# Kernel tuning notes

Hardware: AMD Instinct MI355X
Metric: run time of the kernel (lower is better)

Reference implementation:

```python
import jax, jax.numpy as jnp
import numpy as np

B, E, C = 1024, 512, 16384
MRG, ALPHA, V, K, LAM, TAU = 0.1, 32.0, 100.0, 1.0, 0.1, 1.5


def _l2norm(x):
    # matches torch l2_norm: divide by sqrt(sum(x^2) + 1e-12) row-wise
    n = jnp.sqrt(jnp.sum(x * x, axis=1) + 1e-12)
    return x / n[:, None]


def setup_inputs() -> dict:
    key = jax.random.key(0)
    k1, k2, k3, k4, k5 = jax.random.split(key, 5)
    inputsBatch = _l2norm(jax.random.normal(k1, (B, E), dtype=jnp.float32))
    targetsBatch = jax.random.randint(k2, (B,), 0, C, dtype=jnp.int32)
    # kaiming_normal fan_out on (C, E): std = sqrt(2 / E)
    proxies = jax.random.normal(k3, (C, E), dtype=jnp.float32) * np.sqrt(2.0 / E).astype(np.float32)
    effectiveNum = jax.random.uniform(k4, (C,), dtype=jnp.float32) * 100.0
    learnedSim = jax.random.uniform(k5, (C,), dtype=jnp.float32)
    return {"inputsBatch": inputsBatch, "targetsBatch": targetsBatch,
            "proxies": proxies, "effectiveNum": effectiveNum, "learnedSim": learnedSim}


def reference(inputsBatch, targetsBatch, proxies, effectiveNum, learnedSim):
    nb_classes = proxies.shape[0]
    P = jax.nn.one_hot(targetsBatch, nb_classes, dtype=inputsBatch.dtype)  # [B, C]
    N = 1.0 - P
    proxy_l2 = _l2norm(proxies)
    cos = inputsBatch @ proxy_l2.T  # [B, C]

    classCnt = P.sum(axis=0)                      # [C]
    present = (classCnt > 0).astype(cos.dtype)

    w_base = 1.0 / (1.0 + jnp.log1p(effectiveNum))
    eta = (1.0 + K * (1.0 - learnedSim)) * w_base + LAM
    outlierSim = learnedSim - eta                 # [C]

    # enableFilter=False: mask at positive positions stays 1, so each present
    # class contributes mean(ones)=1 to pos_weight_sum
    pos_weight_sum = jnp.sum(present)

    # negative-position adaptive reweighting (vectorized over the class loop)
    neg_vals = jnp.where(cos < outlierSim[None, :],
                         (1.0 / jnp.maximum(1.0, effectiveNum))[None, :],
                         1.0)                      # [B, C]
    Ncnt = N.sum(axis=0)
    neg_mean = jnp.sum(N * neg_vals, axis=0) / jnp.maximum(Ncnt, 1.0)
    neg_weight_sum = jnp.sum(jnp.where(Ncnt > 0, neg_mean, 0.0))

    mask = jnp.where(N > 0, neg_vals, 1.0)        # 1 at positive entries

    pos_term = jnp.sum(jnp.log1p(jnp.sum(P * jnp.exp(ALPHA * (MRG - cos) * mask), axis=0)))
    neg_term = jnp.sum(jnp.log1p(jnp.sum(N * jnp.exp(ALPHA * (cos + MRG) * mask), axis=0)))

    return pos_term / pos_weight_sum + neg_term / neg_weight_sum
```

## Files before the change

### kernel.cpp

```cpp
#include <hip/hip_runtime.h>
#include <math.h>

#define B_SZ 1024
#define E_SZ 512
#define C_SZ 16384
#define MRG 0.1f
#define ALPHA 32.0f
#define K_HY 1.0f
#define LAM 0.1f

typedef __bf16 bf16;
typedef bf16 bf16x8 __attribute__((ext_vector_type(8)));
typedef float f32x4 __attribute__((ext_vector_type(4)));

__device__ __forceinline__ void async16(const void* g, void* l) {
    __builtin_amdgcn_global_load_lds(
        (const __attribute__((address_space(1))) void*)g,
        (__attribute__((address_space(3))) void*)l,
        16, 0, 0);
}

__global__ void class_scalars(const float* __restrict__ effNum,
                              const float* __restrict__ lSim,
                              float* __restrict__ oSim,
                              float* __restrict__ iEff) {
    int c = blockIdx.x * 256 + threadIdx.x;
    if (c < C_SZ) {
        float en = effNum[c], ls = lSim[c];
        float wb = 1.0f / (1.0f + log1pf(en));
        float eta = (1.0f + K_HY * (1.0f - ls)) * wb + LAM;
        oSim[c] = ls - eta;
        iEff[c] = 1.0f / fmaxf(1.0f, en);
    }
}

__global__ void proxy_norm(const float* __restrict__ proxies, bf16* __restrict__ Pbf) {
    int row = (blockIdx.x * 256 + threadIdx.x) >> 6;
    int lane = threadIdx.x & 63;
    const float* pr = proxies + (size_t)row * E_SZ + lane * 8;
    float4 v0 = *(const float4*)pr;
    float4 v1 = *(const float4*)(pr + 4);
    float ss = v0.x * v0.x + v0.y * v0.y + v0.z * v0.z + v0.w * v0.w +
               v1.x * v1.x + v1.y * v1.y + v1.z * v1.z + v1.w * v1.w;
#pragma unroll
    for (int m = 1; m < 64; m <<= 1) ss += __shfl_xor(ss, m);
    float inv = 1.0f / sqrtf(ss + 1e-12f);
    bf16x8 o;
    o[0] = (bf16)(v0.x * inv); o[1] = (bf16)(v0.y * inv);
    o[2] = (bf16)(v0.z * inv); o[3] = (bf16)(v0.w * inv);
    o[4] = (bf16)(v1.x * inv); o[5] = (bf16)(v1.y * inv);
    o[6] = (bf16)(v1.z * inv); o[7] = (bf16)(v1.w * inv);
    *(bf16x8*)(Pbf + (size_t)row * E_SZ + lane * 8) = o;
}

__global__ void convert_inputs(const float* __restrict__ x, bf16* __restrict__ y) {
    int i = (blockIdx.x * 256 + threadIdx.x) * 8;
    float4 v0 = *(const float4*)(x + i);
    float4 v1 = *(const float4*)(x + i + 4);
    bf16x8 o;
    o[0] = (bf16)v0.x; o[1] = (bf16)v0.y; o[2] = (bf16)v0.z; o[3] = (bf16)v0.w;
    o[4] = (bf16)v1.x; o[5] = (bf16)v1.y; o[6] = (bf16)v1.z; o[7] = (bf16)v1.w;
    *(bf16x8*)(y + i) = o;
}

__global__ void count_targets(const int* __restrict__ tg, int* __restrict__ cnt) {
    int i = blockIdx.x * 256 + threadIdx.x;
    if (i < B_SZ) atomicAdd(&cnt[tg[i]], 1);
}

__global__ __launch_bounds__(256) void gemm_epilogue(
    const bf16* __restrict__ Abf,
    const bf16* __restrict__ Pbf,
    const int* __restrict__ targets,
    const float* __restrict__ oSimA,
    const float* __restrict__ iEffA,
    float* __restrict__ posExp,
    float* __restrict__ negExp,
    float* __restrict__ negVals) {
    __shared__ __align__(16) bf16 Alds[128 * 32];
    __shared__ __align__(16) bf16 Blds[128 * 32];
    __shared__ int tgtLds[128];

    const int tid = threadIdx.x;
    const int wave = tid >> 6, lane = tid & 63;
    const int quad = lane >> 4, l16 = lane & 15;
    const int wRow = (wave >> 1) * 64, wCol = (wave & 1) * 64;
    const int bn0 = blockIdx.x * 128, bm0 = blockIdx.y * 128;

    if (tid < 128) tgtLds[tid] = targets[bm0 + tid];

    f32x4 zero = {0.f, 0.f, 0.f, 0.f};
    f32x4 acc[4][4];
#pragma unroll
    for (int i = 0; i < 4; ++i)
#pragma unroll
        for (int j = 0; j < 4; ++j) acc[i][j] = zero;

    const int ldRow = lane >> 2;
    const int ldK = (lane & 3) * 8;

    const bf16* gA = Abf + (size_t)(bm0 + wave * 32 + ldRow) * E_SZ + ldK;
    const bf16* gB = Pbf + (size_t)(bn0 + wave * 32 + ldRow) * E_SZ + ldK;

    for (int k0 = 0; k0 < E_SZ; k0 += 32) {
        __syncthreads();
#pragma unroll
        for (int j = 0; j < 2; ++j) {
            int chunk = wave * 2 + j;
            async16(gA + (size_t)j * 16 * E_SZ + k0, &Alds[chunk * 512]);
            async16(gB + (size_t)j * 16 * E_SZ + k0, &Blds[chunk * 512]);
        }
        __syncthreads();
        bf16x8 af[4], bff[4];
#pragma unroll
        for (int mi = 0; mi < 4; ++mi)
            af[mi] = *(const bf16x8*)&Alds[(wRow + mi * 16 + l16) * 32 + quad * 8];
#pragma unroll
        for (int ni = 0; ni < 4; ++ni)
            bff[ni] = *(const bf16x8*)&Blds[(wCol + ni * 16 + l16) * 32 + quad * 8];
#pragma unroll
        for (int mi = 0; mi < 4; ++mi)
#pragma unroll
            for (int ni = 0; ni < 4; ++ni)
                acc[mi][ni] = __builtin_amdgcn_mfma_f32_16x16x32_bf16(
                    af[mi], bff[ni], acc[mi][ni], 0, 0, 0);
    }

    int colG[4];
    float oS[4], iE[4];
#pragma unroll
    for (int ni = 0; ni < 4; ++ni) {
        colG[ni] = bn0 + wCol + ni * 16 + l16;
        oS[ni] = oSimA[colG[ni]];
        iE[ni] = iEffA[colG[ni]];
    }
    float negE[4] = {0.f, 0.f, 0.f, 0.f};
    float negV[4] = {0.f, 0.f, 0.f, 0.f};
#pragma unroll
    for (int mi = 0; mi < 4; ++mi) {
#pragma unroll
        for (int r = 0; r < 4; ++r) {
            int rowL = wRow + mi * 16 + quad * 4 + r;
            int tgt = tgtLds[rowL];
#pragma unroll
            for (int ni = 0; ni < 4; ++ni) {
                float cosv = acc[mi][ni][r];
                if (tgt == colG[ni]) {
                    atomicAdd(&posExp[colG[ni]], expf(ALPHA * (MRG - cosv)));
                } else {
                    float nv = (cosv < oS[ni]) ? iE[ni] : 1.0f;
                    negE[ni] += expf(ALPHA * (cosv + MRG) * nv);
                    negV[ni] += nv;
                }
            }
        }
    }
#pragma unroll
    for (int ni = 0; ni < 4; ++ni) {
        float e = negE[ni], v = negV[ni];
        e += __shfl_xor(e, 16); e += __shfl_xor(e, 32);
        v += __shfl_xor(v, 16); v += __shfl_xor(v, 32);
        if (quad == 0) {
            atomicAdd(&negExp[colG[ni]], e);
            atomicAdd(&negVals[colG[ni]], v);
        }
    }
}

__global__ __launch_bounds__(256) void finalize_partial(
    const float* __restrict__ posExp, const float* __restrict__ negExp,
    const float* __restrict__ negVals, const int* __restrict__ cCnt,
    float* __restrict__ acc4) {
    int c = blockIdx.x * 256 + threadIdx.x;
    float pt = log1pf(posExp[c]);
    float nt = log1pf(negExp[c]);
    int cnt = cCnt[c];
    float pws = (cnt > 0) ? 1.0f : 0.0f;
    int Nc = B_SZ - cnt;
    float nws = (Nc > 0) ? negVals[c] / (float)Nc : 0.0f;
#pragma unroll
    for (int m = 1; m < 64; m <<= 1) {
        pt += __shfl_xor(pt, m);
        nt += __shfl_xor(nt, m);
        pws += __shfl_xor(pws, m);
        nws += __shfl_xor(nws, m);
    }
    __shared__ float red[4][4];
    int wv = threadIdx.x >> 6;
    if ((threadIdx.x & 63) == 0) {
        red[wv][0] = pt; red[wv][1] = nt; red[wv][2] = pws; red[wv][3] = nws;
    }
    __syncthreads();
    if (threadIdx.x < 4) {
        float s = red[0][threadIdx.x] + red[1][threadIdx.x] +
                  red[2][threadIdx.x] + red[3][threadIdx.x];
        atomicAdd(&acc4[threadIdx.x], s);
    }
}

__global__ void finalize_out(const float* __restrict__ acc4, float* __restrict__ out) {
    out[0] = acc4[0] / acc4[2] + acc4[1] / acc4[3];
}

extern "C" void kernel_launch(void* const* d_in, const int* in_sizes, int n_in,
                              void* d_out, int out_size, void* d_ws, size_t ws_size,
                              hipStream_t stream) {
    const float* inputs = (const float*)d_in[0];
    const int* targets = (const int*)d_in[1];
    const float* proxies = (const float*)d_in[2];
    const float* effNum = (const float*)d_in[3];
    const float* lSim = (const float*)d_in[4];
    float* out = (float*)d_out;

    bf16* Pbf = (bf16*)d_ws;
    bf16* Abf = Pbf + (size_t)C_SZ * E_SZ;
    float* oSim = (float*)(Abf + (size_t)B_SZ * E_SZ);
    float* iEff = oSim + C_SZ;
    float* posExp = iEff + C_SZ;
    float* negExp = posExp + C_SZ;
    float* negVals = negExp + C_SZ;
    int* cCnt = (int*)(negVals + C_SZ);
    float* acc4 = (float*)(cCnt + C_SZ);

    hipMemsetAsync(posExp, 0, (size_t)4 * C_SZ * sizeof(float) + 4 * sizeof(float), stream);

    class_scalars<<<C_SZ / 256, 256, 0, stream>>>(effNum, lSim, oSim, iEff);
    proxy_norm<<<C_SZ / 4, 256, 0, stream>>>(proxies, Pbf);
    convert_inputs<<<(B_SZ * E_SZ) / (256 * 8), 256, 0, stream>>>(inputs, Abf);
    count_targets<<<B_SZ / 256, 256, 0, stream>>>(targets, cCnt);
    gemm_epilogue<<<dim3(C_SZ / 128, B_SZ / 128), 256, 0, stream>>>(
        Abf, Pbf, targets, oSim, iEff, posExp, negExp, negVals);
    finalize_partial<<<C_SZ / 256, 256, 0, stream>>>(posExp, negExp, negVals, cCnt, acc4);
    finalize_out<<<1, 1, 0, stream>>>(acc4, out);
}
```

Baseline: 131.4 us.

## Fuse prep kernels, double-buffer GEMM LDS tiles, and use fast exp

Folds the class-scalar computation, workspace zeroing, input bf16 conversion and target counting into two launches in place of a memset plus four kernels. This removes launch and memset overhead. The GEMM main loop now double-buffers the A/B LDS tiles with one barrier per K step, so global-to-LDS loads overlap the MFMA work, and it uses a new load/LDS indexing layout. The epilogue swaps expf for __expf, trading some accuracy in the exponentials for speed. Double-buffering doubles LDS use, which could lower occupancy, and with a single barrier per step the correctness of the async loads depends on how that barrier orders them.

```diff
diff --git a/kernel.cpp b/kernel.cpp
--- a/kernel.cpp
+++ b/kernel.cpp
@@ -20,21 +20,42 @@
         16, 0, 0);
 }
 
-__global__ void class_scalars(const float* __restrict__ effNum,
-                              const float* __restrict__ lSim,
-                              float* __restrict__ oSim,
-                              float* __restrict__ iEff) {
+__global__ __launch_bounds__(256) void prep(
+    const float* __restrict__ effNum, const float* __restrict__ lSim,
+    const float* __restrict__ x,
+    float* __restrict__ oSim, float* __restrict__ iEff, bf16* __restrict__ Abf,
+    float* __restrict__ posExp, float* __restrict__ negExp,
+    float* __restrict__ negVals, int* __restrict__ cCnt,
+    float* __restrict__ acc4) {
     int c = blockIdx.x * 256 + threadIdx.x;
-    if (c < C_SZ) {
-        float en = effNum[c], ls = lSim[c];
-        float wb = 1.0f / (1.0f + log1pf(en));
-        float eta = (1.0f + K_HY * (1.0f - ls)) * wb + LAM;
-        oSim[c] = ls - eta;
-        iEff[c] = 1.0f / fmaxf(1.0f, en);
-    }
-}
-
-__global__ void proxy_norm(const float* __restrict__ proxies, bf16* __restrict__ Pbf) {
+    float en = effNum[c], ls = lSim[c];
+    float wb = 1.0f / (1.0f + log1pf(en));
+    float eta = (1.0f + K_HY * (1.0f - ls)) * wb + LAM;
+    oSim[c] = ls - eta;
+    iEff[c] = 1.0f / fmaxf(1.0f, en);
+    posExp[c] = 0.f; negExp[c] = 0.f; negVals[c] = 0.f; cCnt[c] = 0;
+    if (c < 8) acc4[c] = 0.f;
+    const float* xp = x + (size_t)c * 32;
+    bf16* yp = Abf + (size_t)c * 32;
+#pragma unroll
+    for (int j = 0; j < 4; ++j) {
+        float4 v0 = *(const float4*)(xp + j * 8);
+        float4 v1 = *(const float4*)(xp + j * 8 + 4);
+        bf16x8 o;
+        o[0] = (bf16)v0.x; o[1] = (bf16)v0.y; o[2] = (bf16)v0.z; o[3] = (bf16)v0.w;
+        o[4] = (bf16)v1.x; o[5] = (bf16)v1.y; o[6] = (bf16)v1.z; o[7] = (bf16)v1.w;
+        *(bf16x8*)(yp + j * 8) = o;
+    }
+}
+
+__global__ __launch_bounds__(256) void proxy_norm(
+    const float* __restrict__ proxies, bf16* __restrict__ Pbf,
+    const int* __restrict__ tg, int* __restrict__ cCnt) {
+    if (blockIdx.x >= 4096) {
+        int i = (blockIdx.x - 4096) * 256 + threadIdx.x;
+        atomicAdd(&cCnt[tg[i]], 1);
+        return;
+    }
     int row = (blockIdx.x * 256 + threadIdx.x) >> 6;
     int lane = threadIdx.x & 63;
     const float* pr = proxies + (size_t)row * E_SZ + lane * 8;
@@ -51,21 +72,6 @@
     o[4] = (bf16)(v1.x * inv); o[5] = (bf16)(v1.y * inv);
     o[6] = (bf16)(v1.z * inv); o[7] = (bf16)(v1.w * inv);
     *(bf16x8*)(Pbf + (size_t)row * E_SZ + lane * 8) = o;
-}
-
-__global__ void convert_inputs(const float* __restrict__ x, bf16* __restrict__ y) {
-    int i = (blockIdx.x * 256 + threadIdx.x) * 8;
-    float4 v0 = *(const float4*)(x + i);
-    float4 v1 = *(const float4*)(x + i + 4);
-    bf16x8 o;
-    o[0] = (bf16)v0.x; o[1] = (bf16)v0.y; o[2] = (bf16)v0.z; o[3] = (bf16)v0.w;
-    o[4] = (bf16)v1.x; o[5] = (bf16)v1.y; o[6] = (bf16)v1.z; o[7] = (bf16)v1.w;
-    *(bf16x8*)(y + i) = o;
-}
-
-__global__ void count_targets(const int* __restrict__ tg, int* __restrict__ cnt) {
-    int i = blockIdx.x * 256 + threadIdx.x;
-    if (i < B_SZ) atomicAdd(&cnt[tg[i]], 1);
 }
 
 __global__ __launch_bounds__(256) void gemm_epilogue(
@@ -77,8 +83,8 @@
     float* __restrict__ posExp,
     float* __restrict__ negExp,
     float* __restrict__ negVals) {
-    __shared__ __align__(16) bf16 Alds[128 * 32];
-    __shared__ __align__(16) bf16 Blds[128 * 32];
+    __shared__ __align__(16) bf16 Alds[2][128 * 32];
+    __shared__ __align__(16) bf16 Blds[2][128 * 32];
     __shared__ int tgtLds[128];
 
     const int tid = threadIdx.x;
@@ -89,51 +95,56 @@
 
     if (tid < 128) tgtLds[tid] = targets[bm0 + tid];
 
-    f32x4 zero = {0.f, 0.f, 0.f, 0.f};
-    f32x4 acc[4][4];
-#pragma unroll
-    for (int i = 0; i < 4; ++i)
-#pragma unroll
-        for (int j = 0; j < 4; ++j) acc[i][j] = zero;
-
-    const int ldRow = lane >> 2;
-    const int ldK = (lane & 3) * 8;
-
-    const bf16* gA = Abf + (size_t)(bm0 + wave * 32 + ldRow) * E_SZ + ldK;
-    const bf16* gB = Pbf + (size_t)(bn0 + wave * 32 + ldRow) * E_SZ + ldK;
-
-    for (int k0 = 0; k0 < E_SZ; k0 += 32) {
-        __syncthreads();
-#pragma unroll
-        for (int j = 0; j < 2; ++j) {
-            int chunk = wave * 2 + j;
-            async16(gA + (size_t)j * 16 * E_SZ + k0, &Alds[chunk * 512]);
-            async16(gB + (size_t)j * 16 * E_SZ + k0, &Blds[chunk * 512]);
-        }
-        __syncthreads();
-        bf16x8 af[4], bff[4];
-#pragma unroll
-        for (int mi = 0; mi < 4; ++mi)
-            af[mi] = *(const bf16x8*)&Alds[(wRow + mi * 16 + l16) * 32 + quad * 8];
-#pragma unroll
-        for (int ni = 0; ni < 4; ++ni)
-            bff[ni] = *(const bf16x8*)&Blds[(wCol + ni * 16 + l16) * 32 + quad * 8];
-#pragma unroll
-        for (int mi = 0; mi < 4; ++mi)
-#pragma unroll
-            for (int ni = 0; ni < 4; ++ni)
-                acc[mi][ni] = __builtin_amdgcn_mfma_f32_16x16x32_bf16(
-                    af[mi], bff[ni], acc[mi][ni], 0, 0, 0);
-    }
-
-    int colG[4];
-    float oS[4], iE[4];
+    const bf16* gA = Abf + (size_t)(bm0 + wave * 32 + l16) * E_SZ + quad * 8;
+    const bf16* gB = Pbf + (size_t)(bn0 + wave * 32 + l16) * E_SZ + quad * 8;
+
+    int colG[4]; float oS[4], iE[4];
 #pragma unroll
     for (int ni = 0; ni < 4; ++ni) {
         colG[ni] = bn0 + wCol + ni * 16 + l16;
         oS[ni] = oSimA[colG[ni]];
         iE[ni] = iEffA[colG[ni]];
     }
+
+    f32x4 zero = {0.f, 0.f, 0.f, 0.f};
+    f32x4 acc[4][4];
+#pragma unroll
+    for (int i = 0; i < 4; ++i)
+#pragma unroll
+        for (int j = 0; j < 4; ++j) acc[i][j] = zero;
+
+#define STAGE(K0, BUF)                                                        \
+    {                                                                         \
+        _Pragma("unroll")                                                     \
+        for (int j = 0; j < 2; ++j) {                                         \
+            int chunk = wave * 2 + j;                                         \
+            async16(gA + (size_t)j * 16 * E_SZ + (K0), &Alds[BUF][chunk * 512]); \
+            async16(gB + (size_t)j * 16 * E_SZ + (K0), &Blds[BUF][chunk * 512]); \
+        }                                                                     \
+    }
+
+    STAGE(0, 0)
+#pragma unroll
+    for (int kk = 0; kk < 16; ++kk) {
+        __syncthreads();
+        if (kk < 15) STAGE((kk + 1) * 32, (kk + 1) & 1)
+        const int bsel = kk & 1;
+        bf16x8 af[4], bff[4];
+#pragma unroll
+        for (int mi = 0; mi < 4; ++mi)
+            af[mi] = *(const bf16x8*)&Alds[bsel][((wRow >> 4) + mi) * 512 + quad * 128 + l16 * 8];
+#pragma unroll
+        for (int ni = 0; ni < 4; ++ni)
+            bff[ni] = *(const bf16x8*)&Blds[bsel][((wCol >> 4) + ni) * 512 + quad * 128 + l16 * 8];
+#pragma unroll
+        for (int mi = 0; mi < 4; ++mi)
+#pragma unroll
+            for (int ni = 0; ni < 4; ++ni)
+                acc[mi][ni] = __builtin_amdgcn_mfma_f32_16x16x32_bf16(
+                    af[mi], bff[ni], acc[mi][ni], 0, 0, 0);
+    }
+#undef STAGE
+
     float negE[4] = {0.f, 0.f, 0.f, 0.f};
     float negV[4] = {0.f, 0.f, 0.f, 0.f};
 #pragma unroll
@@ -146,10 +157,10 @@
             for (int ni = 0; ni < 4; ++ni) {
                 float cosv = acc[mi][ni][r];
                 if (tgt == colG[ni]) {
-                    atomicAdd(&posExp[colG[ni]], expf(ALPHA * (MRG - cosv)));
+                    atomicAdd(&posExp[colG[ni]], __expf(ALPHA * (MRG - cosv)));
                 } else {
                     float nv = (cosv < oS[ni]) ? iE[ni] : 1.0f;
-                    negE[ni] += expf(ALPHA * (cosv + MRG) * nv);
+                    negE[ni] += __expf(ALPHA * (cosv + MRG) * nv);
                     negV[ni] += nv;
                 }
             }
@@ -222,12 +233,9 @@
     int* cCnt = (int*)(negVals + C_SZ);
     float* acc4 = (float*)(cCnt + C_SZ);
 
-    hipMemsetAsync(posExp, 0, (size_t)4 * C_SZ * sizeof(float) + 4 * sizeof(float), stream);
-
-    class_scalars<<<C_SZ / 256, 256, 0, stream>>>(effNum, lSim, oSim, iEff);
-    proxy_norm<<<C_SZ / 4, 256, 0, stream>>>(proxies, Pbf);
-    convert_inputs<<<(B_SZ * E_SZ) / (256 * 8), 256, 0, stream>>>(inputs, Abf);
-    count_targets<<<B_SZ / 256, 256, 0, stream>>>(targets, cCnt);
+    prep<<<C_SZ / 256, 256, 0, stream>>>(effNum, lSim, inputs, oSim, iEff, Abf,
+                                         posExp, negExp, negVals, cCnt, acc4);
+    proxy_norm<<<4096 + 4, 256, 0, stream>>>(proxies, Pbf, targets, cCnt);
     gemm_epilogue<<<dim3(C_SZ / 128, B_SZ / 128), 256, 0, stream>>>(
         Abf, Pbf, targets, oSim, iEff, posExp, negExp, negVals);
     finalize_partial<<<C_SZ / 256, 256, 0, stream>>>(posExp, negExp, negVals, cCnt, acc4);
```

New measurement: 139.6 us. 6.2% more time.
